# Optimization experiments

Hardware: AMD Instinct MI355X
Metric: run time of the kernel (lower is better)

Reference implementation:

```python
import jax, jax.numpy as jnp
import numpy as np

K = 10  # knn_graph default k
NEG_SLOPE = 0.2


def _knn_idx(x, k):
    # x: (B, N, C) -> idx (B, N, k) of nearest neighbors (excluding self)
    x2 = jnp.sum(x * x, axis=-1)                       # (B, N)
    d = x2[:, :, None] + x2[:, None, :] - 2.0 * jnp.einsum('bnc,bmc->bnm', x, x)
    _, idx = jax.lax.top_k(-d, k + 1)                  # smallest distances
    return idx[:, :, 1:]                               # drop self


def _edge_conv(x, W, s, t, k):
    # x: (B, N, C); W: (O, 2C); s,t: (O,) folded BN scale/bias
    idx = _knn_idx(x, k)                               # (B, N, k)
    neigh = jax.vmap(lambda xb, ib: xb[ib])(x, idx)    # (B, N, k, C)
    xi = jnp.broadcast_to(x[:, :, None, :], neigh.shape)
    edge = jnp.concatenate([neigh - xi, xi], axis=-1)  # (B, N, k, 2C)
    h = jnp.einsum('bnkc,oc->bnko', edge, W) * s + t
    h = jnp.where(h >= 0, h, NEG_SLOPE * h)            # LeakyReLU(0.2)
    return jnp.max(h, axis=2)                          # max over neighbors -> (B, N, O)


def setup_inputs() -> dict:
    key = jax.random.key(0)
    ks = jax.random.split(key, 32)
    B, N = 8, 2048
    NC = 3
    def w(k_, shape):
        fan_in = shape[-1]
        return jax.random.normal(k_, shape, jnp.float32) * (1.0 / np.sqrt(fan_in))
    def sb(k_, c):  # positive scale, small bias
        k1, k2 = jax.random.split(k_)
        return (jax.random.uniform(k1, (c,), jnp.float32, 0.5, 1.5),
                jax.random.normal(k2, (c,), jnp.float32) * 0.1)
    points = jax.random.normal(ks[0], (B, N, 3), jnp.float32)
    W1 = w(ks[1], (64, 6));    s1, t1 = sb(ks[2], 64)
    W2 = w(ks[3], (64, 128));  s2, t2 = sb(ks[4], 64)
    W3 = w(ks[5], (128, 128)); s3, t3 = sb(ks[6], 128)
    W4 = w(ks[7], (256, 256)); s4, t4 = sb(ks[8], 256)
    W5 = w(ks[9], (1024, 512)); s5, t5 = sb(ks[10], 1024)
    Wf1 = w(ks[11], (512, 1024)); sf1, tf1 = sb(ks[12], 512)
    Wf2 = w(ks[13], (256, 512)); bf2 = jax.random.normal(ks[14], (256,), jnp.float32) * 0.02
    sf2, tf2 = sb(ks[15], 256)
    Wf3 = w(ks[16], (NC, 256)); bf3 = jax.random.normal(ks[17], (NC,), jnp.float32) * 0.02
    return {
        'points': points,
        'W1': W1, 's1': s1, 't1': t1,
        'W2': W2, 's2': s2, 't2': t2,
        'W3': W3, 's3': s3, 't3': t3,
        'W4': W4, 's4': s4, 't4': t4,
        'W5': W5, 's5': s5, 't5': t5,
        'Wf1': Wf1, 'sf1': sf1, 'tf1': tf1,
        'Wf2': Wf2, 'bf2': bf2, 'sf2': sf2, 'tf2': tf2,
        'Wf3': Wf3, 'bf3': bf3,
    }


def reference(points, W1, s1, t1, W2, s2, t2, W3, s3, t3, W4, s4, t4,
              W5, s5, t5, Wf1, sf1, tf1, Wf2, bf2, sf2, tf2, Wf3, bf3):
    lrelu = lambda h: jnp.where(h >= 0, h, NEG_SLOPE * h)
    out1 = _edge_conv(points, W1, s1, t1, K)   # (B, N, 64)
    out2 = _edge_conv(out1, W2, s2, t2, K)     # (B, N, 64)
    out3 = _edge_conv(out2, W3, s3, t3, K)     # (B, N, 128)
    out4 = _edge_conv(out3, W4, s4, t4, K)     # (B, N, 256)
    x = jnp.concatenate([out1, out2, out3, out4], axis=-1)  # (B, N, 512)
    h = lrelu(jnp.einsum('bnc,oc->bno', x, W5) * s5 + t5)   # (B, N, 1024)
    h = jnp.max(h, axis=1)                                  # global max pool -> (B, 1024)
    h = lrelu((h @ Wf1.T) * sf1 + tf1)                      # (B, 512); dropout=identity (eval)
    h = lrelu((h @ Wf2.T + bf2) * sf2 + tf2)                # (B, 256)
    return h @ Wf3.T + bf3                                  # (B, num_classes)
```

## Files before the change

### kernel.cpp

```cpp
#include <hip/hip_runtime.h>
#include <hip/hip_bf16.h>


#define NEG 0.2f
#define FMAX 3.402823466e+38f
#define KINIT32 0xFFFFFFFFu

typedef __hip_bfloat16 bf16;
typedef __attribute__((ext_vector_type(8))) short s8v;
typedef __attribute__((ext_vector_type(4))) float f32x4;
typedef unsigned long long u64;

#define BB 8
#define NN 2048
#define BNTOT (BB * NN)
#define NPART 4

#define OFF_NORMS ((size_t)0)
#define OFF_PART (OFF_NORMS + BNTOT)
#define OFF_POOLED (OFF_PART + 8 * 1024 * 32)
#define OFF_H1 (OFF_POOLED + 8 * 1024)
#define OFF_H2 (OFF_H1 + 8 * 512)
#define WSF_TOTAL (OFF_H2 + 8 * 256)

#define WB1 0
#define WB2 4096
#define WB3 12288
#define WB4 28672
#define WTOT 94208

__device__ float g_ws_f[WSF_TOTAL];
__device__ float g_G[(size_t)8 * BNTOT * 64];
__device__ u64 g_pk[(size_t)BNTOT * NPART * 10];
__device__ int g_flag;
__device__ unsigned short g_hi[(size_t)BNTOT * 512];
__device__ unsigned short g_lo[(size_t)BNTOT * 512];
__device__ unsigned short g_xhi5[(size_t)BNTOT * 512];
__device__ unsigned short g_xlo5[(size_t)BNTOT * 512];
__device__ unsigned short g_whi[1024 * 512];
__device__ unsigned short g_wlo[1024 * 512];
__device__ unsigned short g_wfh[WTOT];
__device__ unsigned short g_wfl[WTOT];

__device__ __forceinline__ float ldany(const void* p, size_t i, int isb) {
  if (isb) return __bfloat162float(((const bf16*)p)[i]);
  return ((const float*)p)[i];
}

__global__ void probe_kernel(const void* pts) {
  const unsigned* w = (const unsigned*)pts;
  int cnt = 0;
  for (int i = 0; i < 256; ++i) {
    unsigned e2 = (w[i] >> 7) & 0xFF;
    cnt += (e2 >= 110 && e2 <= 135);
  }
  g_flag = (cnt > 128) ? 1 : 0;
}

__global__ void norms_kernel(const void* xraw, int lda, int C, int BN) {
  const int isb = g_flag;
  float* norms = g_ws_f + OFF_NORMS;
  int row = blockIdx.x * (blockDim.x >> 6) + (threadIdx.x >> 6);
  int lane = threadIdx.x & 63;
  if (row >= BN) return;
  float s = 0.f;
  for (int c = lane; c < C; c += 64) {
    float v = ldany(xraw, (size_t)row * lda + c, isb);
    s += v * v;
  }
#pragma unroll
  for (int off = 32; off > 0; off >>= 1) s += __shfl_down(s, off, 64);
  if (lane == 0) norms[row] = s;
}

__global__ void zero_norms() {
  int i = blockIdx.x * blockDim.x + threadIdx.x;
  if (i < BNTOT) g_ws_f[OFF_NORMS + i] = 0.f;
}

__global__ void split_kernel(const void* xraw, int lda, int C,
                             int csh2, int dst, int total) {
  int i = blockIdx.x * blockDim.x + threadIdx.x;
  if (i >= total) return;
  const int isb = g_flag;
  int t = i >> 9, win = i & 511;
  int quad = win >> 7, l16 = (win >> 3) & 15, j = win & 7;
  int ktiles_m1 = (1 << csh2) - 1;
  int rg = t >> csh2, kt = t & ktiles_m1;
  int r = rg * 16 + l16;
  int c = kt * 32 + quad * 8 + j;
  float v = (c < C) ? ldany(xraw, (size_t)r * lda + c, isb) : 0.f;
  bf16 h = __float2bfloat16(v);
  float hf = __bfloat162float(h);
  bf16 l = __float2bfloat16(v - hf);
  unsigned short* H = dst ? g_whi : g_hi;
  unsigned short* L = dst ? g_wlo : g_lo;
  H[i] = *(unsigned short*)&h;
  L[i] = *(unsigned short*)&l;
}

__global__ void split_w(const void* W, int C, int ktsh, int wbase, int whalf,
                        int total) {
  int i = blockIdx.x * blockDim.x + threadIdx.x;
  if (i >= total) return;
  int z = blockIdx.y;
  const int isb = g_flag;
  int t = i >> 9, win = i & 511;
  int quad = win >> 7, l16 = (win >> 3) & 15, j = win & 7;
  int rg = t >> ktsh, kt = t & ((1 << ktsh) - 1);
  int orow = rg * 16 + l16;
  int c = kt * 32 + quad * 8 + j;
  float v = (c < C) ? ldany(W, (size_t)orow * (2 * C) + (size_t)z * C + c, isb) : 0.f;
  bf16 h = __float2bfloat16(v);
  float hf = __bfloat162float(h);
  bf16 l = __float2bfloat16(v - hf);
  g_wfh[wbase + z * whalf + i] = *(unsigned short*)&h;
  g_wfl[wbase + z * whalf + i] = *(unsigned short*)&l;
}

__device__ __forceinline__ void insert10u(unsigned* K, unsigned key) {
  if (key < K[9]) {
    bool prev = true;
#pragma unroll
    for (int s2 = 9; s2 >= 1; --s2) {
      bool sh = key < K[s2 - 1];
      K[s2] = sh ? K[s2 - 1] : (prev ? key : K[s2]);
      prev = sh;
    }
    if (prev) K[0] = key;
  }
}

template <int CPAD>
__global__ __launch_bounds__(256) void knn_gmat(int N, int BN, int wbase, int whalf) {
  constexpr int KT = CPAD >> 5;
  __shared__ __align__(16) float sdbuf[2][64 * 68];
  __shared__ float th_sh[4][64];
  const int tid = threadIdx.x;
  const int wave = tid >> 6, lane = tid & 63;
  const int quad = lane >> 4, l16 = lane & 15;

  if (blockIdx.z >= 4) {
    const int cz = blockIdx.z - 4;
    const int chunk = cz >> 1;
    const int z = cz & 1;
    const int r0 = ((int)blockIdx.y * 32 + (int)blockIdx.x) * 64;
    const int wz = wbase + z * whalf;
    const int wrg0 = chunk * 4;
    f32x4 acc[4];
#pragma unroll
    for (int s = 0; s < 4; ++s) acc[s] = (f32x4){0.f, 0.f, 0.f, 0.f};
    const int arg = (r0 >> 4) + wave;
#pragma unroll
    for (int kt = 0; kt < KT; ++kt) {
      const int abase = (arg * KT + kt) * 512 + lane * 8;
      s8v ah = *(const s8v*)(g_hi + abase);
      s8v al = *(const s8v*)(g_lo + abase);
#pragma unroll
      for (int s = 0; s < 4; ++s) {
        const int woff = wz + ((wrg0 + s) * KT + kt) * 512 + lane * 8;
        s8v bh = *(const s8v*)(g_wfh + woff);
        s8v bl = *(const s8v*)(g_wfl + woff);
        acc[s] = __builtin_amdgcn_mfma_f32_16x16x32_bf16(ah, bh, acc[s], 0, 0, 0);
        acc[s] = __builtin_amdgcn_mfma_f32_16x16x32_bf16(ah, bl, acc[s], 0, 0, 0);
        acc[s] = __builtin_amdgcn_mfma_f32_16x16x32_bf16(al, bh, acc[s], 0, 0, 0);
      }
    }
    float* Gz = g_G + (size_t)(chunk * 2 + z) * BN * 64;
#pragma unroll
    for (int s = 0; s < 4; ++s)
#pragma unroll
      for (int r = 0; r < 4; ++r)
        Gz[(r0 + wave * 16 + quad * 4 + r) * 64 + s * 16 + l16] = acc[s][r];
    return;
  }

  const int b = blockIdx.y;
  const int q0 = blockIdx.x * 64;
  const int part = blockIdx.z;
  const int PN = N / NPART;
  const int partbase = part * PN;
  const int rowb = b * N;
  const float* norms = g_ws_f + OFF_NORMS;

  const int arg = ((rowb + q0) >> 4) + wave;
  s8v ah[KT], al[KT];
#pragma unroll
  for (int kt = 0; kt < KT; ++kt) {
    const int abase = (arg * KT + kt) * 512 + lane * 8;
    ah[kt] = *(const s8v*)(g_hi + abase);
    al[kt] = *(const s8v*)(g_lo + abase);
  }

  const int selfn = q0 + lane;
  const float qn = norms[rowb + selfn];
  unsigned K[10];
#pragma unroll
  for (int i = 0; i < 10; ++i) K[i] = KINIT32;
  th_sh[wave][lane] = FMAX;

  int pb = 0;
  for (int m0 = partbase; m0 < partbase + PN; m0 += 64, pb ^= 1) {
    float nmv[4];
#pragma unroll
    for (int s = 0; s < 4; ++s) nmv[s] = norms[rowb + m0 + s * 16 + l16];
    f32x4 acc[4];
#pragma unroll
    for (int s = 0; s < 4; ++s) acc[s] = (f32x4){0.f, 0.f, 0.f, 0.f};
    const int brg0 = (rowb + m0) >> 4;
    const int btile = brg0 * (KT * 512) + lane * 8;
#pragma unroll
    for (int kt = 0; kt < KT; ++kt) {
#pragma unroll
      for (int s = 0; s < 4; ++s) {
        const int boff = btile + (s * KT + kt) * 512;
        s8v bh = *(const s8v*)(g_hi + boff);
        s8v bl = *(const s8v*)(g_lo + boff);
        acc[s] = __builtin_amdgcn_mfma_f32_16x16x32_bf16(ah[kt], bh, acc[s], 0, 0, 0);
        acc[s] = __builtin_amdgcn_mfma_f32_16x16x32_bf16(ah[kt], bl, acc[s], 0, 0, 0);
        acc[s] = __builtin_amdgcn_mfma_f32_16x16x32_bf16(al[kt], bh, acc[s], 0, 0, 0);
      }
    }
    float* sd = sdbuf[pb];
#pragma unroll
    for (int s = 0; s < 4; ++s) {
      int ml = s * 16 + l16;
#pragma unroll
      for (int r = 0; r < 4; ++r)
        sd[(wave * 16 + quad * 4 + r) * 68 + ml] = nmv[s] - 2.f * acc[s][r];
    }
    __syncthreads();
    float T = fminf(fminf(th_sh[0][lane], th_sh[1][lane]),
                    fminf(th_sh[2][lane], th_sh[3][lane]));
    {
      unsigned tb = K[9] & 0xFFFFFE00u;
      tb = (tb >= 0x7F7FFE00u) ? 0x7F800000u : tb + 0x200u;
      T = fminf(T, __uint_as_float(tb));
    }
    const float Tq = T - qn;
    const int mbase = m0 + wave * 16;
    const int mrelbase = mbase - partbase;
    const float* srow = sd + lane * 68 + wave * 16;
    unsigned pass = 0;
#pragma unroll
    for (int jj = 0; jj < 16; jj += 4) {
      float4 d4 = *(const float4*)(srow + jj);
      pass |= (unsigned)(d4.x <= Tq) << jj;
      pass |= (unsigned)(d4.y <= Tq) << (jj + 1);
      pass |= (unsigned)(d4.z <= Tq) << (jj + 2);
      pass |= (unsigned)(d4.w <= Tq) << (jj + 3);
    }
    if ((unsigned)(selfn - mbase) < 16u) pass &= ~(1u << (selfn - mbase));
    while (pass) {
      int jj = __builtin_ctz(pass);
      pass &= pass - 1;
      float d = fmaxf(srow[jj] + qn, 0.f);
      unsigned key = (__float_as_uint(d) & 0xFFFFFE00u) | (unsigned)(mrelbase + jj);
      insert10u(K, key);
    }
    {
      unsigned tb = K[9] & 0xFFFFFE00u;
      tb = (tb >= 0x7F7FFE00u) ? 0x7F800000u : tb + 0x200u;
      th_sh[wave][lane] = __uint_as_float(tb);
    }
  }
  __syncthreads();
  unsigned* mlist = (unsigned*)sdbuf;
#pragma unroll
  for (int i = 0; i < 10; ++i) mlist[(lane * 4 + wave) * 10 + i] = K[i];
  __syncthreads();
  if (tid < 64) {
    int q = tid;
    int p0 = 0, p1 = 0, p2 = 0, p3 = 0;
    size_t ob = ((size_t)(rowb + q0 + q) * NPART + part) * 10;
    for (int cnt = 0; cnt < 10; ++cnt) {
      unsigned k0 = mlist[(q * 4 + 0) * 10 + p0];
      unsigned k1 = mlist[(q * 4 + 1) * 10 + p1];
      unsigned k2 = mlist[(q * 4 + 2) * 10 + p2];
      unsigned k3 = mlist[(q * 4 + 3) * 10 + p3];
      unsigned bk = k0; int bp = 0;
      if (k1 < bk) { bk = k1; bp = 1; }
      if (k2 < bk) { bk = k2; bp = 2; }
      if (k3 < bk) { bk = k3; bp = 3; }
      if (bp == 0) ++p0; else if (bp == 1) ++p1; else if (bp == 2) ++p2; else ++p3;
      g_pk[ob + cnt] = ((u64)(bk & 0xFFFFFE00u) << 32) |
                       (unsigned)(partbase + (int)(bk & 0x1FFu));
    }
  }
}

__global__ void edge_epi64(const void* s, const void* t, int colbase,
                           int knn_csh2, int norms_mode, int BN, int N) {
  __shared__ u64 kbuf[4][40];
  __shared__ int oidx[4][10];
  const int isb = g_flag;
  int tid = threadIdx.x;
  int p = tid >> 6, o = tid & 63;
  int row = blockIdx.x * 4 + p;
  int chunk = blockIdx.y;
  const float* G1 = g_G + (size_t)(chunk * 2 + 0) * BN * 64;
  const float* G2 = g_G + (size_t)(chunk * 2 + 1) * BN * 64;
  int b = row / N;
  if (o < 40) kbuf[p][o] = g_pk[(size_t)row * 40 + o];
  if (o < 40) {
    u64 myk = kbuf[p][o];
    int rank = 0;
#pragma unroll 8
    for (int j = 0; j < 40; ++j) rank += (kbuf[p][j] < myk);
    if (rank < 10) oidx[p][rank] = (int)(myk & 0xFFFFFFFFu);
  }
  float g1n = G1[row * 64 + o];
  float base = G2[row * 64 + o] - g1n;
  int co = chunk * 64 + o;
  float sv = ldany(s, co, isb), tv = ldany(t, co, isb);
  float mx = -FMAX;
  const int bn64 = b * N * 64;
#pragma unroll
  for (int k = 0; k < 10; ++k) {
    int m = oidx[p][k];
    m = (m < 0) ? 0 : ((m >= N) ? N - 1 : m);
    float h = sv * (G1[bn64 + m * 64 + o] + base) + tv;
    h = (h >= 0.f) ? h : NEG * h;
    mx = fmaxf(mx, h);
  }
  bf16 h16 = __float2bfloat16(mx);
  float hf = __bfloat162float(h16);
  bf16 l16v = __float2bfloat16(mx - hf);
  unsigned short hu = *(unsigned short*)&h16;
  unsigned short lu = *(unsigned short*)&l16v;
  if (knn_csh2 >= 0) {
    int KTL = 1 << knn_csh2;
    int ki = ((row >> 4) * KTL + (co >> 5)) * 512 +
             ((co >> 3) & 3) * 128 + (row & 15) * 8 + (co & 7);
    g_hi[ki] = hu; g_lo[ki] = lu;
  }
  {
    int gc = colbase + co;
    int wi = ((row >> 4) * 16 + (gc >> 5)) * 512 +
             ((gc >> 3) & 3) * 128 + (row & 15) * 8 + (gc & 7);
    g_xhi5[wi] = hu; g_xlo5[wi] = lu;
  }
  if (norms_mode) {
    float ns = mx * mx;
#pragma unroll
    for (int off = 32; off > 0; off >>= 1) ns += __shfl_down(ns, off, 64);
    if (o == 0) {
      if (norms_mode == 1) g_ws_f[OFF_NORMS + row] = ns;
      else atomicAdd(&g_ws_f[OFF_NORMS + row], ns);
    }
  }
}

__global__ __launch_bounds__(256) void w5max_mfma(const void* s5, const void* t5, int N) {
  const int tid = threadIdx.x;
  const int wave = tid >> 6, lane = tid & 63;
  const int quad = lane >> 4, l16 = lane & 15;
  const int b = blockIdx.z;
  const int o0 = blockIdx.y * 64, n0 = blockIdx.x * 256;
  f32x4 acc[4][4];
#pragma unroll
  for (int a = 0; a < 4; ++a)
#pragma unroll
    for (int s = 0; s < 4; ++s) acc[a][s] = (f32x4){0.f, 0.f, 0.f, 0.f};

  const int arg0 = ((b * N + n0) >> 4) + wave * 4;
  const int wrg0 = o0 >> 4;
  for (int kt = 0; kt < 16; ++kt) {
    s8v ah[4], al[4];
#pragma unroll
    for (int a = 0; a < 4; ++a) {
      const int abase = ((arg0 + a) * 16 + kt) * 512 + lane * 8;
      ah[a] = *(const s8v*)(g_xhi5 + abase);
      al[a] = *(const s8v*)(g_xlo5 + abase);
    }
#pragma unroll
    for (int s = 0; s < 4; ++s) {
      const int bbase = ((wrg0 + s) * 16 + kt) * 512 + lane * 8;
      s8v bh = *(const s8v*)(g_whi + bbase);
      s8v bl = *(const s8v*)(g_wlo + bbase);
#pragma unroll
      for (int a = 0; a < 4; ++a) {
        acc[a][s] = __builtin_amdgcn_mfma_f32_16x16x32_bf16(ah[a], bh, acc[a][s], 0, 0, 0);
        acc[a][s] = __builtin_amdgcn_mfma_f32_16x16x32_bf16(ah[a], bl, acc[a][s], 0, 0, 0);
        acc[a][s] = __builtin_amdgcn_mfma_f32_16x16x32_bf16(al[a], bh, acc[a][s], 0, 0, 0);
      }
    }
  }
  __shared__ float red[4][64];
  const int isb = g_flag;
#pragma unroll
  for (int s = 0; s < 4; ++s) {
    float m4 = -FMAX;
#pragma unroll
    for (int a = 0; a < 4; ++a)
#pragma unroll
      for (int r = 0; r < 4; ++r) m4 = fmaxf(m4, acc[a][s][r]);
#pragma unroll
    for (int off = 16; off < 64; off <<= 1) m4 = fmaxf(m4, __shfl_down(m4, off, 64));
    if (quad == 0) red[wave][s * 16 + l16] = m4;
  }
  __syncthreads();
  if (tid < 64) {
    float m = fmaxf(fmaxf(red[0][tid], red[1][tid]), fmaxf(red[2][tid], red[3][tid]));
    int o = o0 + tid;
    float sv = ldany(s5, o, isb), tv = ldany(t5, o, isb);
    float h = sv * m + tv;
    h = (h >= 0.f) ? h : NEG * h;
    g_ws_f[OFF_PART + ((size_t)b * 1024 + o) * 8 + blockIdx.x] = h;
  }
}

__global__ void poolred_kernel() {
  const float* part = g_ws_f + OFF_PART;
  float* pooled = g_ws_f + OFF_POOLED;
  int i = blockIdx.x * blockDim.x + threadIdx.x;
  if (i >= 8 * 1024) return;
  const float* p = part + (size_t)i * 8;
  float m = -FMAX;
#pragma unroll
  for (int j = 0; j < 8; ++j) m = fmaxf(m, p[j]);
  pooled[i] = m;
}

__global__ void fc_kernel(size_t inoff, const void* W, const void* bias,
                          const void* s, const void* t, size_t outoff, int has_out,
                          void* OUTB, int Bb, int IC, int OC, int act) {
  const int isb = g_flag;
  const float* IN = g_ws_f + inoff;
  int gw = (blockIdx.x * blockDim.x + threadIdx.x) >> 6;
  int lane = threadIdx.x & 63;
  if (gw >= Bb * OC) return;
  int b = gw / OC, o = gw % OC;
  const float* in = IN + (size_t)b * IC;
  float acc = 0.f;
  for (int c = lane; c < IC; c += 64) acc += in[c] * ldany(W, (size_t)o * IC + c, isb);
#pragma unroll
  for (int off = 32; off > 0; off >>= 1) acc += __shfl_down(acc, off, 64);
  if (lane == 0) {
    float h = acc;
    if (bias) h += ldany(bias, o, isb);
    if (s) h = h * ldany(s, o, isb) + ldany(t, o, isb);
    if (act) h = (h >= 0.f) ? h : NEG * h;
    if (has_out) g_ws_f[outoff + (size_t)b * OC + o] = h;
    if (OUTB) {
      if (isb) ((bf16*)OUTB)[(size_t)b * OC + o] = __float2bfloat16(h);
      else ((float*)OUTB)[(size_t)b * OC + o] = h;
    }
  }
}

extern "C" void kernel_launch(void* const* d_in, const int* in_sizes, int n_in,
                              void* d_out, int out_size, void* d_ws, size_t ws_size,
                              hipStream_t stream) {
  const int B = 8, N = 2048, BN = B * N;
  const void* points = d_in[0];
  const void *W1 = d_in[1], *s1 = d_in[2], *t1 = d_in[3];
  const void *W2 = d_in[4], *s2 = d_in[5], *t2 = d_in[6];
  const void *W3 = d_in[7], *s3 = d_in[8], *t3 = d_in[9];
  const void *W4 = d_in[10], *s4 = d_in[11], *t4 = d_in[12];
  const void *W5 = d_in[13], *s5 = d_in[14], *t5 = d_in[15];
  const void *Wf1 = d_in[16], *sf1 = d_in[17], *tf1 = d_in[18];
  const void *Wf2 = d_in[19], *bf2 = d_in[20], *sf2 = d_in[21], *tf2 = d_in[22];
  const void *Wf3 = d_in[23], *bf3 = d_in[24];

  probe_kernel<<<1, 1, 0, stream>>>(points);
  split_kernel<<<(1024 * 512) / 256, 256, 0, stream>>>(W5, 512, 512, 4, 1, 1024 * 512);
  split_w<<<dim3(2048 / 256, 2), 256, 0, stream>>>(W1, 3, 0, WB1, 2048, 2048);
  split_w<<<dim3(4096 / 256, 2), 256, 0, stream>>>(W2, 64, 1, WB2, 4096, 4096);
  split_w<<<dim3(8192 / 256, 2), 256, 0, stream>>>(W3, 64, 1, WB3, 8192, 8192);
  split_w<<<dim3(32768 / 256, 2), 256, 0, stream>>>(W4, 128, 2, WB4, 32768, 32768);

  norms_kernel<<<BN / 4, 256, 0, stream>>>(points, 3, 3, BN);
  split_kernel<<<(BN * 32) / 256, 256, 0, stream>>>(points, 3, 3, 0, 0, BN * 32);
  knn_gmat<32><<<dim3(N / 64, B, 4 + 2), 256, 0, stream>>>(N, BN, WB1, 2048);
  edge_epi64<<<dim3(BN / 4, 1), 256, 0, stream>>>(s1, t1, 0, 1, 1, BN, N);
  knn_gmat<64><<<dim3(N / 64, B, 4 + 2), 256, 0, stream>>>(N, BN, WB2, 4096);
  edge_epi64<<<dim3(BN / 4, 1), 256, 0, stream>>>(s2, t2, 64, 1, 1, BN, N);
  knn_gmat<64><<<dim3(N / 64, B, 4 + 4), 256, 0, stream>>>(N, BN, WB3, 8192);
  zero_norms<<<BN / 256, 256, 0, stream>>>();
  edge_epi64<<<dim3(BN / 4, 2), 256, 0, stream>>>(s3, t3, 128, 2, 2, BN, N);
  knn_gmat<128><<<dim3(N / 64, B, 4 + 8), 256, 0, stream>>>(N, BN, WB4, 32768);
  edge_epi64<<<dim3(BN / 4, 4), 256, 0, stream>>>(s4, t4, 256, -1, 0, BN, N);
  w5max_mfma<<<dim3(8, 16, 8), 256, 0, stream>>>(s5, t5, N);
  poolred_kernel<<<32, 256, 0, stream>>>();
  fc_kernel<<<(8 * 512 * 64) / 256, 256, 0, stream>>>(OFF_POOLED, Wf1, nullptr, sf1, tf1, OFF_H1, 1, nullptr, 8, 1024, 512, 1);
  fc_kernel<<<(8 * 256 * 64) / 256, 256, 0, stream>>>(OFF_H1, Wf2, bf2, sf2, tf2, OFF_H2, 1, nullptr, 8, 512, 256, 1);
  fc_kernel<<<6, 256, 0, stream>>>(OFF_H2, Wf3, bf3, nullptr, nullptr, 0, 0, d_out, 8, 256, 3, 0);
}
```

Baseline: 481.2 us.

## Move per-point weight GEMM into knn blocks via atomic work queue

Removes the separate grid z-slices that computed the edge-conv weight projection G and instead has each kNN wave, after finishing its top-k work, pull 16-row GEMM tiles from a global atomic counter until all tiles are done. The intent is to fill idle tail time in the kNN blocks with the projection work and to shrink the launch grid. Counters are reset in the probe kernel once per forward pass. This adds one atomic per tile per wave and makes load balance depend on dynamic scheduling.

```diff
diff --git a/kernel.cpp b/kernel.cpp
--- a/kernel.cpp
+++ b/kernel.cpp
@@ -33,6 +33,7 @@
 __device__ float g_G[(size_t)8 * BNTOT * 64];
 __device__ u64 g_pk[(size_t)BNTOT * NPART * 10];
 __device__ int g_flag;
+__device__ unsigned g_wq[4];
 __device__ unsigned short g_hi[(size_t)BNTOT * 512];
 __device__ unsigned short g_lo[(size_t)BNTOT * 512];
 __device__ unsigned short g_xhi5[(size_t)BNTOT * 512];
@@ -55,6 +56,7 @@
     cnt += (e2 >= 110 && e2 <= 135);
   }
   g_flag = (cnt > 128) ? 1 : 0;
+  g_wq[0] = 0; g_wq[1] = 0; g_wq[2] = 0; g_wq[3] = 0;
 }
 
 __global__ void norms_kernel(const void* xraw, int lda, int C, int BN) {
@@ -132,49 +134,14 @@
 }
 
 template <int CPAD>
-__global__ __launch_bounds__(256) void knn_gmat(int N, int BN, int wbase, int whalf) {
+__global__ __launch_bounds__(256) void knn_gmat(int N, int BN, int wbase,
+                                                int whalf, int wqi, int ngmat) {
   constexpr int KT = CPAD >> 5;
   __shared__ __align__(16) float sdbuf[2][64 * 68];
   __shared__ float th_sh[4][64];
   const int tid = threadIdx.x;
   const int wave = tid >> 6, lane = tid & 63;
   const int quad = lane >> 4, l16 = lane & 15;
-
-  if (blockIdx.z >= 4) {
-    const int cz = blockIdx.z - 4;
-    const int chunk = cz >> 1;
-    const int z = cz & 1;
-    const int r0 = ((int)blockIdx.y * 32 + (int)blockIdx.x) * 64;
-    const int wz = wbase + z * whalf;
-    const int wrg0 = chunk * 4;
-    f32x4 acc[4];
-#pragma unroll
-    for (int s = 0; s < 4; ++s) acc[s] = (f32x4){0.f, 0.f, 0.f, 0.f};
-    const int arg = (r0 >> 4) + wave;
-#pragma unroll
-    for (int kt = 0; kt < KT; ++kt) {
-      const int abase = (arg * KT + kt) * 512 + lane * 8;
-      s8v ah = *(const s8v*)(g_hi + abase);
-      s8v al = *(const s8v*)(g_lo + abase);
-#pragma unroll
-      for (int s = 0; s < 4; ++s) {
-        const int woff = wz + ((wrg0 + s) * KT + kt) * 512 + lane * 8;
-        s8v bh = *(const s8v*)(g_wfh + woff);
-        s8v bl = *(const s8v*)(g_wfl + woff);
-        acc[s] = __builtin_amdgcn_mfma_f32_16x16x32_bf16(ah, bh, acc[s], 0, 0, 0);
-        acc[s] = __builtin_amdgcn_mfma_f32_16x16x32_bf16(ah, bl, acc[s], 0, 0, 0);
-        acc[s] = __builtin_amdgcn_mfma_f32_16x16x32_bf16(al, bh, acc[s], 0, 0, 0);
-      }
-    }
-    float* Gz = g_G + (size_t)(chunk * 2 + z) * BN * 64;
-#pragma unroll
-    for (int s = 0; s < 4; ++s)
-#pragma unroll
-      for (int r = 0; r < 4; ++r)
-        Gz[(r0 + wave * 16 + quad * 4 + r) * 64 + s * 16 + l16] = acc[s][r];
-    return;
-  }
-
   const int b = blockIdx.y;
   const int q0 = blockIdx.x * 64;
   const int part = blockIdx.z;
@@ -287,6 +254,42 @@
                        (unsigned)(partbase + (int)(bk & 0x1FFu));
     }
   }
+  for (;;) {
+    int t;
+    if (lane == 0) t = (int)atomicAdd(&g_wq[wqi], 1u);
+    t = __shfl(t, 0, 64);
+    if (t >= ngmat) break;
+    const int wrow = t & 1023;
+    const int rest = t >> 10;
+    const int chunk = rest >> 1;
+    const int z = rest & 1;
+    const int wz = wbase + z * whalf;
+    const int wrg0 = chunk * 4;
+    f32x4 gacc[4];
+#pragma unroll
+    for (int s = 0; s < 4; ++s) gacc[s] = (f32x4){0.f, 0.f, 0.f, 0.f};
+#pragma unroll
+    for (int kt = 0; kt < KT; ++kt) {
+      const int gab = (wrow * KT + kt) * 512 + lane * 8;
+      s8v gah = *(const s8v*)(g_hi + gab);
+      s8v gal = *(const s8v*)(g_lo + gab);
+#pragma unroll
+      for (int s = 0; s < 4; ++s) {
+        const int woff = wz + ((wrg0 + s) * KT + kt) * 512 + lane * 8;
+        s8v bh = *(const s8v*)(g_wfh + woff);
+        s8v bl = *(const s8v*)(g_wfl + woff);
+        gacc[s] = __builtin_amdgcn_mfma_f32_16x16x32_bf16(gah, bh, gacc[s], 0, 0, 0);
+        gacc[s] = __builtin_amdgcn_mfma_f32_16x16x32_bf16(gah, bl, gacc[s], 0, 0, 0);
+        gacc[s] = __builtin_amdgcn_mfma_f32_16x16x32_bf16(gal, bh, gacc[s], 0, 0, 0);
+      }
+    }
+    float* Gz = g_G + (size_t)(chunk * 2 + z) * BN * 64;
+#pragma unroll
+    for (int s = 0; s < 4; ++s)
+#pragma unroll
+      for (int r = 0; r < 4; ++r)
+        Gz[(wrow * 16 + quad * 4 + r) * 64 + s * 16 + l16] = gacc[s][r];
+  }
 }
 
 __global__ void edge_epi64(const void* s, const void* t, int colbase,
@@ -472,14 +475,14 @@
 
   norms_kernel<<<BN / 4, 256, 0, stream>>>(points, 3, 3, BN);
   split_kernel<<<(BN * 32) / 256, 256, 0, stream>>>(points, 3, 3, 0, 0, BN * 32);
-  knn_gmat<32><<<dim3(N / 64, B, 4 + 2), 256, 0, stream>>>(N, BN, WB1, 2048);
+  knn_gmat<32><<<dim3(N / 64, B, NPART), 256, 0, stream>>>(N, BN, WB1, 2048, 0, 2048);
   edge_epi64<<<dim3(BN / 4, 1), 256, 0, stream>>>(s1, t1, 0, 1, 1, BN, N);
-  knn_gmat<64><<<dim3(N / 64, B, 4 + 2), 256, 0, stream>>>(N, BN, WB2, 4096);
+  knn_gmat<64><<<dim3(N / 64, B, NPART), 256, 0, stream>>>(N, BN, WB2, 4096, 1, 2048);
   edge_epi64<<<dim3(BN / 4, 1), 256, 0, stream>>>(s2, t2, 64, 1, 1, BN, N);
-  knn_gmat<64><<<dim3(N / 64, B, 4 + 4), 256, 0, stream>>>(N, BN, WB3, 8192);
+  knn_gmat<64><<<dim3(N / 64, B, NPART), 256, 0, stream>>>(N, BN, WB3, 8192, 2, 4096);
   zero_norms<<<BN / 256, 256, 0, stream>>>();
   edge_epi64<<<dim3(BN / 4, 2), 256, 0, stream>>>(s3, t3, 128, 2, 2, BN, N);
-  knn_gmat<128><<<dim3(N / 64, B, 4 + 8), 256, 0, stream>>>(N, BN, WB4, 32768);
+  knn_gmat<128><<<dim3(N / 64, B, NPART), 256, 0, stream>>>(N, BN, WB4, 32768, 3, 8192);
   edge_epi64<<<dim3(BN / 4, 4), 256, 0, stream>>>(s4, t4, 256, -1, 0, BN, N);
   w5max_mfma<<<dim3(8, 16, 8), 256, 0, stream>>>(s5, t5, N);
   poolred_kernel<<<32, 256, 0, stream>>>();
```

Measured after the change: 792.5 us. 64.7% more time.
